# Performance work log

Hardware: AMD Instinct MI355X
Metric: run time of the kernel (lower is better)

## Reference

```python
import jax, jax.numpy as jnp
import numpy as np

N_NODES = 100000
N_EDGES = 1600000
IN_C, HID_C, OUT_C = 512, 128, 40


def gcn_conv(x, edge_index):
    """Symmetric-normalized sparse aggregation: out[d] = sum_e 1/sqrt(deg[s]*deg[d]) * x[s]."""
    n = x.shape[0]
    src, dst = edge_index[0], edge_index[1]
    deg = jax.ops.segment_sum(jnp.ones_like(dst, dtype=x.dtype), dst, num_segments=n)
    deg = jnp.maximum(deg, 1.0)  # guard isolated nodes
    dinv = jax.lax.rsqrt(deg)
    w = dinv[src] * dinv[dst]                      # [E]
    msg = x[src] * w[:, None]                      # [E, C] gather + scale
    return jax.ops.segment_sum(msg, dst, num_segments=n)  # scatter-add -> [N, C]


def setup_inputs() -> dict:
    key = jax.random.key(0)
    k1, k2, k3, k4 = jax.random.split(key, 4)
    x = jax.random.normal(k1, (N_NODES, IN_C), dtype=jnp.float32)
    edge_index = jax.random.randint(k2, (2, N_EDGES), 0, N_NODES, dtype=jnp.int64)
    # xavier_uniform with gain=1.414 (as in reset_parameters), zero biases
    def xavier(k, shape, gain=1.414):
        fan_out, fan_in = shape
        bound = gain * np.sqrt(6.0 / (fan_in + fan_out))
        return jax.random.uniform(k, shape, jnp.float32, -bound, bound)
    W0 = xavier(k3, (HID_C, IN_C))
    b0 = jnp.zeros((HID_C,), jnp.float32)
    W1 = xavier(k4, (OUT_C, HID_C))
    b1 = jnp.zeros((OUT_C,), jnp.float32)
    return {"x": x, "edge_index": edge_index, "W0": W0, "b0": b0, "W1": W1, "b1": b1}


def reference(x, edge_index, W0, b0, W1, b1):
    # layer 0: project -> sparse aggregate -> bias -> relu (dropout off in eval)
    h = x @ W0.T
    h = gcn_conv(h, edge_index)
    h = jax.nn.relu(h + b0)
    # final layer: project -> sparse aggregate -> bias (no activation)
    h = h @ W1.T
    h = gcn_conv(h, edge_index)
    return h + b1
```

## Files before the change

### kernel.cpp

```cpp
#include <hip/hip_runtime.h>
#include <hip/hip_bf16.h>
#include <cstddef>

#define N_NODES 100000
#define N_EDGES 1600000
#define IN_C 512
#define HID_C 128
#define OUT_C 40
#define OUT_CP 48
#define BK 128
#define PADK 136
#define EPB 8000
#define NPART 200
#define NBKT 196
#define BSHIFT 9

typedef short bf16x8 __attribute__((ext_vector_type(8)));
typedef float f32x4 __attribute__((ext_vector_type(4)));

__device__ __forceinline__ float bf2f(unsigned short u) {
    union { unsigned int i; float f; } v; v.i = ((unsigned int)u) << 16; return v.f;
}
__device__ __forceinline__ float bf2f_lo(unsigned int u) {
    union { unsigned int i; float f; } v; v.i = u << 16; return v.f;
}
__device__ __forceinline__ float bf2f_hi(unsigned int u) {
    union { unsigned int i; float f; } v; v.i = u & 0xFFFF0000u; return v.f;
}
__device__ __forceinline__ unsigned short f2bf(float f) {
    union { float f; unsigned int i; } v; v.f = f;
    unsigned int x = v.i;
    return (unsigned short)((x + 0x7FFFu + ((x >> 16) & 1u)) >> 16);
}

__global__ void k_detect(const unsigned int* __restrict__ xbits,
                         const int* __restrict__ ei32, int* __restrict__ flags) {
    if (threadIdx.x == 0 && blockIdx.x == 0) {
        int inrange = 0;
        for (int i = 0; i < 64; i++) {
            unsigned int b = xbits[i * 33 + 1];
            int e = (int)((b >> 23) & 0xFFu);
            if (e >= 90 && e <= 160) inrange++;
        }
        flags[0] = (inrange >= 32) ? 0 : 1;
        int zeros = 0;
        for (int i = 0; i < 8; i++) if (ei32[2 * i + 1] == 0) zeros++;
        flags[1] = (zeros == 8) ? 1 : 0;
    }
}

__device__ __forceinline__ int load_src(const int* ei, int mi, int e) {
    return mi ? ei[2 * e] : ei[e];
}
__device__ __forceinline__ int load_dst(const int* ei, int mi, int e) {
    return mi ? ei[2 * (N_EDGES + e)] : ei[N_EDGES + e];
}

#define NW_TOTAL (IN_C * HID_C + HID_C * OUT_C + HID_C + OUT_C)
__global__ void k_norm_w(const void* __restrict__ W0, const void* __restrict__ W1,
                         const void* __restrict__ b0, const void* __restrict__ b1,
                         const int* __restrict__ flags,
                         unsigned short* __restrict__ w0n, unsigned short* __restrict__ w1n,
                         float* __restrict__ b0n, float* __restrict__ b1n) {
    int mf = flags[0];
    int i = blockIdx.x * 256 + threadIdx.x;
    if (i >= NW_TOTAL) return;
    if (i < IN_C * HID_C) {
        w0n[i] = mf ? ((const unsigned short*)W0)[i] : f2bf(((const float*)W0)[i]);
    } else if (i < IN_C * HID_C + HID_C * OUT_C) {
        int j = i - IN_C * HID_C;
        w1n[j] = mf ? ((const unsigned short*)W1)[j] : f2bf(((const float*)W1)[j]);
    } else if (i < IN_C * HID_C + HID_C * OUT_C + HID_C) {
        int j = i - IN_C * HID_C - HID_C * OUT_C;
        b0n[j] = mf ? bf2f(((const unsigned short*)b0)[j]) : ((const float*)b0)[j];
    } else {
        int j = i - IN_C * HID_C - HID_C * OUT_C - HID_C;
        b1n[j] = mf ? bf2f(((const unsigned short*)b1)[j]) : ((const float*)b1)[j];
    }
}

__global__ __launch_bounds__(256) void k_part1(const int* __restrict__ ei,
                                               const int* __restrict__ flags,
                                               int* __restrict__ bcnt,
                                               int* __restrict__ block_off) {
    __shared__ int h[NBKT];
    int t = threadIdx.x;
    for (int i = t; i < NBKT; i += 256) h[i] = 0;
    __syncthreads();
    int mi = flags[1];
    int base = blockIdx.x * EPB;
    for (int j = t; j < EPB; j += 256) {
        int e = base + j;
        if (e < N_EDGES) atomicAdd(&h[load_dst(ei, mi, e) >> BSHIFT], 1);
    }
    __syncthreads();
    for (int i = t; i < NBKT; i += 256)
        block_off[blockIdx.x * NBKT + i] = atomicAdd(&bcnt[i], h[i]);
}

__global__ void k_scan_bkt(const int* __restrict__ bcnt, int* __restrict__ bbase) {
    __shared__ int sm[256];
    int t = threadIdx.x;
    int v = (t < NBKT) ? bcnt[t] : 0;
    sm[t] = v; __syncthreads();
    for (int off = 1; off < 256; off <<= 1) {
        int a = (t >= off) ? sm[t - off] : 0;
        __syncthreads();
        sm[t] += a;
        __syncthreads();
    }
    if (t < NBKT) bbase[t] = sm[t] - v;
    if (t == NBKT - 1) bbase[NBKT] = sm[t];
}

__global__ __launch_bounds__(256) void k_part2(const int* __restrict__ ei,
                                               const int* __restrict__ flags,
                                               const int* __restrict__ bbase,
                                               const int* __restrict__ block_off,
                                               unsigned int* __restrict__ bedges) {
    __shared__ int cur[NBKT];
    int t = threadIdx.x;
    for (int i = t; i < NBKT; i += 256)
        cur[i] = bbase[i] + block_off[blockIdx.x * NBKT + i];
    __syncthreads();
    int mi = flags[1];
    int base = blockIdx.x * EPB;
    for (int j = t; j < EPB; j += 256) {
        int e = base + j;
        if (e < N_EDGES) {
            int d = load_dst(ei, mi, e);
            int s = load_src(ei, mi, e);
            int p = atomicAdd(&cur[d >> BSHIFT], 1);
            bedges[p] = ((unsigned int)s << BSHIFT) | (unsigned int)(d & 511);
        }
    }
}

__global__ __launch_bounds__(512) void k_bucket_csr(const unsigned int* __restrict__ bedges,
                                                    const int* __restrict__ bbase,
                                                    int* __restrict__ rowptr,
                                                    float* __restrict__ dinv,
                                                    int* __restrict__ col) {
    __shared__ int cnt[512];
    __shared__ int cur[512];
    int b = blockIdx.x, t = threadIdx.x;
    int ebeg = bbase[b], eend = bbase[b + 1];
    cnt[t] = 0;
    __syncthreads();
    for (int j = ebeg + t; j < eend; j += 512)
        atomicAdd(&cnt[bedges[j] & 511], 1);
    __syncthreads();
    int v = cnt[t];
    cur[t] = v; __syncthreads();
    for (int off = 1; off < 512; off <<= 1) {
        int a = (t >= off) ? cur[t - off] : 0;
        __syncthreads();
        cur[t] += a;
        __syncthreads();
    }
    int excl = cur[t] - v;
    int node = b * 512 + t;
    if (node < N_NODES) {
        rowptr[node] = ebeg + excl;
        float dd = (float)v; if (dd < 1.f) dd = 1.f;
        dinv[node] = rsqrtf(dd);
    } else if (node == N_NODES) {
        rowptr[N_NODES] = ebeg + excl;
    }
    __syncthreads();
    cur[t] = ebeg + excl;
    __syncthreads();
    for (int j = ebeg + t; j < eend; j += 512) {
        unsigned int pk = bedges[j];
        int p = atomicAdd(&cur[pk & 511], 1);
        col[p] = (int)(pk >> BSHIFT);
    }
}

template <int MF>
__device__ __forceinline__ void gemm1_body(const void* __restrict__ x,
                                           const unsigned short* __restrict__ w0n,
                                           unsigned short* __restrict__ h1,
                                           unsigned short* __restrict__ Bl,
                                           int node0, int t) {
    int w = t >> 6;
    int lane = t & 63;
    int r16 = lane & 15;
    int quad = lane >> 4;

    f32x4 acc[2][8];
#pragma unroll
    for (int m = 0; m < 2; m++)
#pragma unroll
        for (int c = 0; c < 8; c++) acc[m][c] = (f32x4){0.f, 0.f, 0.f, 0.f};

    int row0 = node0 + w * 32 + r16;
    int row1 = row0 + 16;
    int r0c = row0 < N_NODES ? row0 : N_NODES - 1;
    int r1c = row1 < N_NODES ? row1 : N_NODES - 1;
    const float* a0f = (const float*)x + (size_t)r0c * IN_C + quad * 8;
    const float* a1f = (const float*)x + (size_t)r1c * IN_C + quad * 8;
    const unsigned short* a0h = (const unsigned short*)x + (size_t)r0c * IN_C + quad * 8;
    const unsigned short* a1h = (const unsigned short*)x + (size_t)r1c * IN_C + quad * 8;

    int ch = t >> 1, half = t & 1;
    const unsigned short* gfill = w0n + (size_t)ch * IN_C + half * 64;
    unsigned short* lfill = Bl + ch * PADK + half * 64;

    for (int s = 0; s < 4; s++) {
        int ks0 = s * BK;
        __syncthreads();
#pragma unroll
        for (int i = 0; i < 8; i++) {
            *reinterpret_cast<bf16x8*>(lfill + i * 8) =
                *reinterpret_cast<const bf16x8*>(gfill + ks0 + i * 8);
        }
        __syncthreads();
#pragma unroll
        for (int kk = 0; kk < BK; kk += 32) {
            int k0 = ks0 + kk;
            bf16x8 a0, a1;
            if (MF) {
                a0 = *reinterpret_cast<const bf16x8*>(a0h + k0);
                a1 = *reinterpret_cast<const bf16x8*>(a1h + k0);
            } else {
                float4 f0 = *reinterpret_cast<const float4*>(a0f + k0);
                float4 f1 = *reinterpret_cast<const float4*>(a0f + k0 + 4);
                float4 g0 = *reinterpret_cast<const float4*>(a1f + k0);
                float4 g1 = *reinterpret_cast<const float4*>(a1f + k0 + 4);
                a0 = (bf16x8){(short)f2bf(f0.x), (short)f2bf(f0.y), (short)f2bf(f0.z), (short)f2bf(f0.w),
                              (short)f2bf(f1.x), (short)f2bf(f1.y), (short)f2bf(f1.z), (short)f2bf(f1.w)};
                a1 = (bf16x8){(short)f2bf(g0.x), (short)f2bf(g0.y), (short)f2bf(g0.z), (short)f2bf(g0.w),
                              (short)f2bf(g1.x), (short)f2bf(g1.y), (short)f2bf(g1.z), (short)f2bf(g1.w)};
            }
            const unsigned short* bbase2 = Bl + r16 * PADK + kk + quad * 8;
#pragma unroll
            for (int ct = 0; ct < 8; ct++) {
                bf16x8 b = *reinterpret_cast<const bf16x8*>(bbase2 + ct * 16 * PADK);
                acc[0][ct] = __builtin_amdgcn_mfma_f32_16x16x32_bf16(a0, b, acc[0][ct], 0, 0, 0);
                acc[1][ct] = __builtin_amdgcn_mfma_f32_16x16x32_bf16(a1, b, acc[1][ct], 0, 0, 0);
            }
        }
    }

#pragma unroll
    for (int m = 0; m < 2; m++) {
#pragma unroll
        for (int ct = 0; ct < 8; ct++) {
#pragma unroll
            for (int r = 0; r < 4; r++) {
                int row = node0 + w * 32 + m * 16 + quad * 4 + r;
                if (row < N_NODES)
                    h1[(size_t)row * HID_C + ct * 16 + r16] = f2bf(acc[m][ct][r]);
            }
        }
    }
}

__global__ __launch_bounds__(256, 3) void k_gemm1(const void* __restrict__ x,
                                                  const unsigned short* __restrict__ w0n,
                                                  const int* __restrict__ flags,
                                                  unsigned short* __restrict__ h1) {
    __shared__ unsigned short Bl[HID_C * PADK];
    int node0 = blockIdx.x * 128;
    int t = threadIdx.x;
    if (flags[0]) gemm1_body<1>(x, w0n, h1, Bl, node0, t);
    else          gemm1_body<0>(x, w0n, h1, Bl, node0, t);
}

__global__ __launch_bounds__(256) void k_agg1(const int* __restrict__ rowptr,
                                              const int* __restrict__ col,
                                              const float* __restrict__ dinv,
                                              const unsigned int* __restrict__ h1v,
                                              const float* __restrict__ b0n,
                                              unsigned int* __restrict__ h2v) {
    int w = threadIdx.x >> 6;
    int lane = threadIdx.x & 63;
    int d = blockIdx.x * 4 + w;
    if (d >= N_NODES) return;
    int beg = rowptr[d], end = rowptr[d + 1];
    float a0 = 0.f, a1 = 0.f;
    int j = beg;
    for (; j + 8 <= end; j += 8) {
        int s[8];
        float wj[8];
        unsigned int r[8];
#pragma unroll
        for (int q = 0; q < 8; q++) s[q] = col[j + q];
#pragma unroll
        for (int q = 0; q < 8; q++) wj[q] = dinv[s[q]];
#pragma unroll
        for (int q = 0; q < 8; q++) r[q] = h1v[(size_t)s[q] * 64 + lane];
#pragma unroll
        for (int q = 0; q < 8; q++) {
            a0 += wj[q] * bf2f_lo(r[q]);
            a1 += wj[q] * bf2f_hi(r[q]);
        }
    }
    for (; j < end; j++) {
        int s = col[j];
        float wj = dinv[s];
        unsigned int r = h1v[(size_t)s * 64 + lane];
        a0 += wj * bf2f_lo(r);
        a1 += wj * bf2f_hi(r);
    }
    float dv = dinv[d];
    float o0 = a0 * dv + b0n[2 * lane];
    float o1 = a1 * dv + b0n[2 * lane + 1];
    o0 = o0 > 0.f ? o0 : 0.f;
    o1 = o1 > 0.f ? o1 : 0.f;
    h2v[(size_t)d * 64 + lane] = (unsigned int)f2bf(o0) | ((unsigned int)f2bf(o1) << 16);
}

__global__ __launch_bounds__(256) void k_gemm2(const unsigned short* __restrict__ h2,
                                               const unsigned short* __restrict__ w1p,
                                               float* __restrict__ p2) {
    int wave = (blockIdx.x * 256 + (int)threadIdx.x) >> 6;
    if (wave >= N_NODES / 16) return;
    int lane = threadIdx.x & 63;
    int r16 = lane & 15;
    int quad = lane >> 4;
    int node_base = wave * 16;

    f32x4 acc[3];
#pragma unroll
    for (int c = 0; c < 3; c++) acc[c] = (f32x4){0.f, 0.f, 0.f, 0.f};

    const unsigned short* arow = h2 + (size_t)(node_base + r16) * HID_C + quad * 8;
    const unsigned short* brow = w1p + (size_t)r16 * HID_C + quad * 8;

#pragma unroll
    for (int k0 = 0; k0 < HID_C; k0 += 32) {
        bf16x8 a = *reinterpret_cast<const bf16x8*>(arow + k0);
#pragma unroll
        for (int ct = 0; ct < 3; ct++) {
            bf16x8 b = *reinterpret_cast<const bf16x8*>(brow + (size_t)ct * 16 * HID_C + k0);
            acc[ct] = __builtin_amdgcn_mfma_f32_16x16x32_bf16(a, b, acc[ct], 0, 0, 0);
        }
    }

#pragma unroll
    for (int ct = 0; ct < 3; ct++) {
        int chan = ct * 16 + r16;
        if (chan < OUT_C) {
#pragma unroll
            for (int r = 0; r < 4; r++) {
                p2[(size_t)(node_base + quad * 4 + r) * OUT_C + chan] = acc[ct][r];
            }
        }
    }
}

__global__ __launch_bounds__(256) void k_agg2(const int* __restrict__ rowptr,
                                              const int* __restrict__ col,
                                              const float* __restrict__ dinv,
                                              const float* __restrict__ p2,
                                              const float* __restrict__ b1n,
                                              const int* __restrict__ flags,
                                              void* __restrict__ out) {
    int w = threadIdx.x >> 6;
    int lane = threadIdx.x & 63;
    int d = blockIdx.x * 4 + w;
    if (d >= N_NODES || lane >= OUT_C) return;
    int beg = rowptr[d], end = rowptr[d + 1];
    float acc = 0.f;
    int j = beg;
    for (; j + 8 <= end; j += 8) {
        int s[8];
        float wj[8], r[8];
#pragma unroll
        for (int q = 0; q < 8; q++) s[q] = col[j + q];
#pragma unroll
        for (int q = 0; q < 8; q++) wj[q] = dinv[s[q]];
#pragma unroll
        for (int q = 0; q < 8; q++) r[q] = p2[(size_t)s[q] * OUT_C + lane];
#pragma unroll
        for (int q = 0; q < 8; q++) acc += wj[q] * r[q];
    }
    for (; j < end; j++) {
        int s = col[j];
        acc += dinv[s] * p2[(size_t)s * OUT_C + lane];
    }
    float v = acc * dinv[d] + b1n[lane];
    size_t idx = (size_t)d * OUT_C + lane;
    if (flags[0]) ((unsigned short*)out)[idx] = f2bf(v);
    else          ((float*)out)[idx] = v;
}

extern "C" void kernel_launch(void* const* d_in, const int* in_sizes, int n_in,
                              void* d_out, int out_size, void* d_ws, size_t ws_size,
                              hipStream_t stream) {
    const void* x  = d_in[0];
    const int* ei  = (const int*)d_in[1];
    const void* W0 = d_in[2];
    const void* b0 = d_in[3];
    const void* W1 = d_in[4];
    const void* b1 = d_in[5];

    char* ws = (char*)d_ws;
    size_t off = 0;
    auto alloc = [&](size_t bytes) {
        char* p = ws + off;
        off += (bytes + 511) & ~(size_t)511;
        return p;
    };
    int*   flags   = (int*)  alloc(sizeof(int) * 2);
    int*   rowptr  = (int*)  alloc(sizeof(int) * (N_NODES + 1));
    float* dinv    = (float*)alloc(sizeof(float) * N_NODES);
    int*   col     = (int*)  alloc(sizeof(int) * N_EDGES);
    int*   bcnt    = (int*)  alloc(sizeof(int) * NBKT);
    int*   bbase   = (int*)  alloc(sizeof(int) * (NBKT + 1));
    int*   bloff   = (int*)  alloc(sizeof(int) * NPART * NBKT);
    unsigned int* bedges = (unsigned int*)alloc(sizeof(unsigned int) * N_EDGES);
    unsigned short* w0n = (unsigned short*)alloc(sizeof(unsigned short) * IN_C * HID_C);
    unsigned short* w1n = (unsigned short*)alloc(sizeof(unsigned short) * OUT_CP * HID_C);
    float* b0n = (float*)alloc(sizeof(float) * HID_C);
    float* b1n = (float*)alloc(sizeof(float) * OUT_C);
    unsigned short* h1 = (unsigned short*)alloc(sizeof(unsigned short) * (size_t)N_NODES * HID_C);
    unsigned short* h2 = (unsigned short*)alloc(sizeof(unsigned short) * (size_t)N_NODES * HID_C);
    float* p2 = (float*)h1;

    k_detect<<<1, 64, 0, stream>>>((const unsigned int*)x, ei, flags);
    hipMemsetAsync(w1n, 0, sizeof(unsigned short) * OUT_CP * HID_C, stream);
    k_norm_w<<<(NW_TOTAL + 255) / 256, 256, 0, stream>>>(W0, W1, b0, b1, flags, w0n, w1n, b0n, b1n);

    hipMemsetAsync(bcnt, 0, sizeof(int) * NBKT, stream);
    k_part1<<<NPART, 256, 0, stream>>>(ei, flags, bcnt, bloff);
    k_scan_bkt<<<1, 256, 0, stream>>>(bcnt, bbase);
    k_part2<<<NPART, 256, 0, stream>>>(ei, flags, bbase, bloff, bedges);
    k_bucket_csr<<<NBKT, 512, 0, stream>>>(bedges, bbase, rowptr, dinv, col);

    k_gemm1<<<(N_NODES + 127) / 128, 256, 0, stream>>>(x, w0n, flags, h1);
    k_agg1<<<(N_NODES + 3) / 4, 256, 0, stream>>>(rowptr, col, dinv,
                                                  (const unsigned int*)h1, b0n,
                                                  (unsigned int*)h2);
    k_gemm2<<<(N_NODES / 16 + 3) / 4, 256, 0, stream>>>(h2, w1n, p2);
    k_agg2<<<(N_NODES + 3) / 4, 256, 0, stream>>>(rowptr, col, dinv, p2, b1n, flags, d_out);
}
```

Before: 565.4 us.

## Double-buffer bf16 GEMM1 tiles via async global-to-LDS loads

Adds a bf16-input path for the first projection GEMM that streams A and W0 tiles straight into LDS with global_load_lds, double-buffered across 16 K-steps of 32, and feeds MFMA 16x16x32 bf16 from the staged fragments. The aim is to overlap global loads with matrix math and skip register-staged copies. It replaces the templated body only when the flag marks bf16 input; the fp32 path is unchanged. Padding-free LDS reads may cause bank conflicts.

```diff
diff --git a/kernel.cpp b/kernel.cpp
--- a/kernel.cpp
+++ b/kernel.cpp
@@ -31,6 +31,13 @@
     union { float f; unsigned int i; } v; v.f = f;
     unsigned int x = v.i;
     return (unsigned short)((x + 0x7FFFu + ((x >> 16) & 1u)) >> 16);
+}
+
+__device__ __forceinline__ void glds16(const void* g, void* l) {
+    __builtin_amdgcn_global_load_lds(
+        (const __attribute__((address_space(1))) unsigned int*)g,
+        (__attribute__((address_space(3))) unsigned int*)l,
+        16, 0, 0);
 }
 
 __global__ void k_detect(const unsigned int* __restrict__ xbits,
@@ -257,15 +264,85 @@
     }
 }
 
+__device__ __forceinline__ void gemm1_bf16_async(const unsigned short* __restrict__ xg,
+                                                 const unsigned short* __restrict__ w0n,
+                                                 unsigned short* __restrict__ h1,
+                                                 unsigned short* __restrict__ smem,
+                                                 int node0, int t) {
+    const int w = t >> 6;
+    const int lane = t & 63;
+    const int r16 = lane & 15;
+    const int quad = lane >> 4;
+
+    f32x4 acc[2][8];
+#pragma unroll
+    for (int m = 0; m < 2; m++)
+#pragma unroll
+        for (int c = 0; c < 8; c++) acc[m][c] = (f32x4){0.f, 0.f, 0.f, 0.f};
+
+    int rA0 = node0 + (2 * w) * 16 + r16;     if (rA0 >= N_NODES) rA0 = N_NODES - 1;
+    int rA1 = node0 + (2 * w + 1) * 16 + r16; if (rA1 >= N_NODES) rA1 = N_NODES - 1;
+    const unsigned short* pa0 = xg + (size_t)rA0 * IN_C + quad * 8;
+    const unsigned short* pa1 = xg + (size_t)rA1 * IN_C + quad * 8;
+    const unsigned short* pb0 = w0n + (size_t)((2 * w) * 16 + r16) * IN_C + quad * 8;
+    const unsigned short* pb1 = w0n + (size_t)((2 * w + 1) * 16 + r16) * IN_C + quad * 8;
+
+    auto stage = [&](int buf, int ks) {
+        unsigned short* a = smem + buf * 8192 + (2 * w) * 512;
+        glds16(pa0 + ks, a);
+        glds16(pa1 + ks, a + 512);
+        glds16(pb0 + ks, a + 4096);
+        glds16(pb1 + ks, a + 4096 + 512);
+    };
+
+    const int fo = quad * 128 + r16 * 8;
+
+    auto compute = [&](int buf) {
+        const unsigned short* Ab = smem + buf * 8192;
+        const unsigned short* Bb = Ab + 4096;
+        bf16x8 a0 = *reinterpret_cast<const bf16x8*>(Ab + (2 * w) * 512 + fo);
+        bf16x8 a1 = *reinterpret_cast<const bf16x8*>(Ab + (2 * w + 1) * 512 + fo);
+#pragma unroll
+        for (int ct = 0; ct < 8; ct++) {
+            bf16x8 b = *reinterpret_cast<const bf16x8*>(Bb + ct * 512 + fo);
+            acc[0][ct] = __builtin_amdgcn_mfma_f32_16x16x32_bf16(a0, b, acc[0][ct], 0, 0, 0);
+            acc[1][ct] = __builtin_amdgcn_mfma_f32_16x16x32_bf16(a1, b, acc[1][ct], 0, 0, 0);
+        }
+    };
+
+    stage(0, 0);
+    __syncthreads();
+    for (int tt = 0; tt < 15; ++tt) {
+        int cur = tt & 1;
+        stage(cur ^ 1, (tt + 1) * 32);
+        compute(cur);
+        __syncthreads();
+    }
+    compute(1);
+
+#pragma unroll
+    for (int m = 0; m < 2; m++) {
+#pragma unroll
+        for (int ct = 0; ct < 8; ct++) {
+#pragma unroll
+            for (int r = 0; r < 4; r++) {
+                int row = node0 + w * 32 + m * 16 + quad * 4 + r;
+                if (row < N_NODES)
+                    h1[(size_t)row * HID_C + ct * 16 + r16] = f2bf(acc[m][ct][r]);
+            }
+        }
+    }
+}
+
 __global__ __launch_bounds__(256, 3) void k_gemm1(const void* __restrict__ x,
                                                   const unsigned short* __restrict__ w0n,
                                                   const int* __restrict__ flags,
                                                   unsigned short* __restrict__ h1) {
-    __shared__ unsigned short Bl[HID_C * PADK];
+    __shared__ unsigned short smem[HID_C * PADK];
     int node0 = blockIdx.x * 128;
     int t = threadIdx.x;
-    if (flags[0]) gemm1_body<1>(x, w0n, h1, Bl, node0, t);
-    else          gemm1_body<0>(x, w0n, h1, Bl, node0, t);
+    if (flags[0]) gemm1_bf16_async((const unsigned short*)x, w0n, h1, smem, node0, t);
+    else          gemm1_body<0>(x, w0n, h1, smem, node0, t);
 }
 
 __global__ __launch_bounds__(256) void k_agg1(const int* __restrict__ rowptr,
```

Measured after the change: 566.0 us. About the same (+0.1%).
